# Performance work log

Hardware: AMD Instinct MI355X
Metric: run time of the kernel (lower is better)

The kernel has to match this reference:

```python
import jax, jax.numpy as jnp
import numpy as np

DIM = 64


def setup_inputs() -> dict:
    key = jax.random.key(0)
    k1, k2, k3 = jax.random.split(key, 3)
    x = jax.random.normal(k1, (65536, DIM), dtype=jnp.float32)
    alpha = jax.random.uniform(k2, (), dtype=jnp.float32)
    beta = jax.random.uniform(k3, (), dtype=jnp.float32)
    return {"x": x, "alpha": alpha, "beta": beta}


def reference(x, alpha, beta):
    # Static upper-triangular index pairs (i < j), same as triu(...,1).nonzero()
    iu, ju = jnp.triu_indices(DIM, k=1)
    e = jnp.exp(-alpha * x)                 # [B, dim]
    # a[b, p] = exp(-alpha*x_i) - exp(-alpha*x_j) for each pair p=(i,j), i<j.
    # Equivalent to building the dense [B, dim, dim] tensor and gathering triu.
    a = e[..., iu] - e[..., ju]             # [B, dim*(dim-1)/2]
    log_vander = jnp.sum(jnp.log(jnp.abs(a)), axis=-1)  # [B]
    return 2.0 * (-beta * jnp.sum(x, axis=-1) + log_vander)
```

## Files before the change

kernel.cpp:

```cpp
#include <hip/hip_runtime.h>

#define RS 66

typedef float v2f __attribute__((ext_vector_type(2)));

__device__ __forceinline__ float lgc(float p) {
  return __builtin_amdgcn_logf(__builtin_fmaxf(__builtin_fabsf(p), 1e-37f));
}

__device__ __forceinline__ void ld8v(const float* p, v2f (&r)[4]) {
#pragma unroll
  for (int k = 0; k < 4; ++k) r[k] = *reinterpret_cast<const v2f*>(p + 2 * k);
}

__device__ __forceinline__ void row8p(float a, const v2f (&ej)[4], float& acc) {
  v2f aa = {a, a};
  v2f d0 = aa - ej[0], d1 = aa - ej[1], d2 = aa - ej[2], d3 = aa - ej[3];
  v2f p = (d0 * d1) * (d2 * d3);
  acc += lgc(p.x * p.y);
}

__device__ __forceinline__ void crossp(const v2f (&ei)[4], const v2f (&ej)[4],
                                       float& a0, float& a1) {
  row8p(ei[0].x, ej, a0); row8p(ei[0].y, ej, a1);
  row8p(ei[1].x, ej, a0); row8p(ei[1].y, ej, a1);
  row8p(ei[2].x, ej, a0); row8p(ei[2].y, ej, a1);
  row8p(ei[3].x, ej, a0); row8p(ei[3].y, ej, a1);
}

__device__ __forceinline__ void diag(const v2f (&v)[4], float& a0, float& a1) {
  float e0 = v[0].x, e1 = v[0].y, e2 = v[1].x, e3 = v[1].y;
  float e4 = v[2].x, e5 = v[2].y, e6 = v[3].x, e7 = v[3].y;
  a0 += lgc((((e0 - e1) * (e0 - e2)) * ((e0 - e3) * (e0 - e4))) *
            (((e0 - e5) * (e0 - e6)) * ((e0 - e7) * (e1 - e2))));
  a1 += lgc((((e1 - e3) * (e1 - e4)) * ((e1 - e5) * (e1 - e6))) *
            (((e1 - e7) * (e2 - e3)) * ((e2 - e4) * (e2 - e5))));
  a0 += lgc((((e2 - e6) * (e2 - e7)) * ((e3 - e4) * (e3 - e5))) *
            (((e3 - e6) * (e3 - e7)) * ((e4 - e5) * (e4 - e6))));
  a1 += lgc(((e4 - e7) * (e5 - e6)) * ((e5 - e7) * (e6 - e7)));
}

__global__ __launch_bounds__(512, 8) void vander_kernel(
    const float* __restrict__ x, const float* __restrict__ alpha,
    const float* __restrict__ beta, float* __restrict__ out) {
  __shared__ float e_lds[64 * RS];
  __shared__ float xsum[64 * 9];
  __shared__ float ps[64 * 9];

  const int tid = threadIdx.x;
  const float c = -alpha[0] * 1.44269504088896340736f;

  {
    const int r = tid >> 3, cc = tid & 7;
    const float4* xp = reinterpret_cast<const float4*>(
        x + ((size_t)blockIdx.x * 64 + r) * 64 + cc * 8);
    float4 u = xp[0], v = xp[1];
    float* ew = &e_lds[r * RS + cc * 8];
    float2 t;
    t.x = __builtin_amdgcn_exp2f(c * u.x); t.y = __builtin_amdgcn_exp2f(c * u.y);
    *reinterpret_cast<float2*>(ew + 0) = t;
    t.x = __builtin_amdgcn_exp2f(c * u.z); t.y = __builtin_amdgcn_exp2f(c * u.w);
    *reinterpret_cast<float2*>(ew + 2) = t;
    t.x = __builtin_amdgcn_exp2f(c * v.x); t.y = __builtin_amdgcn_exp2f(c * v.y);
    *reinterpret_cast<float2*>(ew + 4) = t;
    t.x = __builtin_amdgcn_exp2f(c * v.z); t.y = __builtin_amdgcn_exp2f(c * v.w);
    *reinterpret_cast<float2*>(ew + 6) = t;
    xsum[r * 9 + cc] = ((u.x + u.y) + (u.z + u.w)) + ((v.x + v.y) + (v.z + v.w));
  }
  __syncthreads();

  const int lane = tid & 63;
  const int w = tid >> 6;
  const float* myrow = &e_lds[lane * RS];

  v2f ei[4], ej[4];
  ld8v(myrow + w * 8, ei);
  float a0 = 0.f, a1 = 0.f;

  ld8v(myrow + ((w + 1) & 7) * 8, ej);
  crossp(ei, ej, a0, a1);
  ld8v(myrow + ((w + 2) & 7) * 8, ej);
  crossp(ei, ej, a0, a1);
  ld8v(myrow + ((w + 3) & 7) * 8, ej);
  crossp(ei, ej, a0, a1);

  ld8v(myrow + ((w + 4) & 7) * 8, ej);
  if (w < 4) {
    row8p(ei[0].x, ej, a0); row8p(ei[0].y, ej, a1);
    row8p(ei[1].x, ej, a0); row8p(ei[1].y, ej, a1);
  } else {
    row8p(ej[2].x, ei, a0); row8p(ej[2].y, ei, a1);
    row8p(ej[3].x, ei, a0); row8p(ej[3].y, ei, a1);
  }
  diag(ei, a0, a1);

  ps[lane * 9 + w] = a0 + a1;
  __syncthreads();

  if (w == 0) {
    const float* pp = &ps[lane * 9];
    const float* xq = &xsum[lane * 9];
    float lv = ((pp[0] + pp[1]) + (pp[2] + pp[3])) + ((pp[4] + pp[5]) + (pp[6] + pp[7]));
    float xs = ((xq[0] + xq[1]) + (xq[2] + xq[3])) + ((xq[4] + xq[5]) + (xq[6] + xq[7]));
    out[blockIdx.x * 64 + lane] =
        2.0f * (-beta[0] * xs + 0.69314718055994530942f * lv);
  }
}

extern "C" void kernel_launch(void* const* d_in, const int* in_sizes, int n_in,
                              void* d_out, int out_size, void* d_ws, size_t ws_size,
                              hipStream_t stream) {
  const float* x = (const float*)d_in[0];
  const float* alpha = (const float*)d_in[1];
  const float* beta = (const float*)d_in[2];
  float* out = (float*)d_out;
  int nrows = in_sizes[0] / 64;
  int grid = nrows / 64;
  hipLaunchKernelGGL(vander_kernel, dim3(grid), dim3(512), 0, stream,
                     x, alpha, beta, out);
}
```

Before: 71.09 us.

## Replace per-product log with exponent/mantissa accumulation and a single final log

Groups pair differences into 16-element products and accumulates each product's exponent bits as an integer and its mantissa in [1,2) as a running float product. Per thread, only one log2 of the mantissa product is taken at the end, instead of one log per 8-element product. This cuts the transcendental instruction count roughly in half or more and replaces it with cheap integer and bit operations. The trade-offs are that 16-term products can underflow or overflow, which the 1e-37 clamp masks, and that the mantissa product chain (up to about 8 multiplies across two accumulators) may lose precision or overflow.

```diff
diff --git a/kernel.cpp b/kernel.cpp
--- a/kernel.cpp
+++ b/kernel.cpp
@@ -4,8 +4,11 @@
 
 typedef float v2f __attribute__((ext_vector_type(2)));
 
-__device__ __forceinline__ float lgc(float p) {
-  return __builtin_amdgcn_logf(__builtin_fmaxf(__builtin_fabsf(p), 1e-37f));
+__device__ __forceinline__ void acc16(float p, int& ea, float& m) {
+  p = __builtin_fmaxf(__builtin_fabsf(p), 1e-37f);
+  const int b = __float_as_int(p);
+  ea += (b >> 23);
+  m *= __int_as_float((b & 0x007FFFFF) | 0x3F800000);
 }
 
 __device__ __forceinline__ void ld8v(const float* p, v2f (&r)[4]) {
@@ -13,31 +16,37 @@
   for (int k = 0; k < 4; ++k) r[k] = *reinterpret_cast<const v2f*>(p + 2 * k);
 }
 
-__device__ __forceinline__ void row8p(float a, const v2f (&ej)[4], float& acc) {
-  v2f aa = {a, a};
-  v2f d0 = aa - ej[0], d1 = aa - ej[1], d2 = aa - ej[2], d3 = aa - ej[3];
-  v2f p = (d0 * d1) * (d2 * d3);
-  acc += lgc(p.x * p.y);
+__device__ __forceinline__ void row16(float a, float b, const v2f (&ej)[4],
+                                      int& ea, float& m) {
+  v2f aa = {a, a}, bb = {b, b};
+  v2f qa = ((aa - ej[0]) * (aa - ej[1])) * ((aa - ej[2]) * (aa - ej[3]));
+  v2f qb = ((bb - ej[0]) * (bb - ej[1])) * ((bb - ej[2]) * (bb - ej[3]));
+  v2f q = qa * qb;
+  acc16(q.x * q.y, ea, m);
 }
 
 __device__ __forceinline__ void crossp(const v2f (&ei)[4], const v2f (&ej)[4],
-                                       float& a0, float& a1) {
-  row8p(ei[0].x, ej, a0); row8p(ei[0].y, ej, a1);
-  row8p(ei[1].x, ej, a0); row8p(ei[1].y, ej, a1);
-  row8p(ei[2].x, ej, a0); row8p(ei[2].y, ej, a1);
-  row8p(ei[3].x, ej, a0); row8p(ei[3].y, ej, a1);
+                                       int& e0, float& m0, int& e1, float& m1) {
+  row16(ei[0].x, ei[0].y, ej, e0, m0);
+  row16(ei[1].x, ei[1].y, ej, e1, m1);
+  row16(ei[2].x, ei[2].y, ej, e0, m0);
+  row16(ei[3].x, ei[3].y, ej, e1, m1);
 }
 
-__device__ __forceinline__ void diag(const v2f (&v)[4], float& a0, float& a1) {
-  float e0 = v[0].x, e1 = v[0].y, e2 = v[1].x, e3 = v[1].y;
-  float e4 = v[2].x, e5 = v[2].y, e6 = v[3].x, e7 = v[3].y;
-  a0 += lgc((((e0 - e1) * (e0 - e2)) * ((e0 - e3) * (e0 - e4))) *
-            (((e0 - e5) * (e0 - e6)) * ((e0 - e7) * (e1 - e2))));
-  a1 += lgc((((e1 - e3) * (e1 - e4)) * ((e1 - e5) * (e1 - e6))) *
-            (((e1 - e7) * (e2 - e3)) * ((e2 - e4) * (e2 - e5))));
-  a0 += lgc((((e2 - e6) * (e2 - e7)) * ((e3 - e4) * (e3 - e5))) *
-            (((e3 - e6) * (e3 - e7)) * ((e4 - e5) * (e4 - e6))));
-  a1 += lgc(((e4 - e7) * (e5 - e6)) * ((e5 - e7) * (e6 - e7)));
+__device__ __forceinline__ void diag(const v2f (&v)[4], int& e0, float& m0,
+                                     int& e1, float& m1) {
+  float a = v[0].x, b = v[0].y, c = v[1].x, d = v[1].y;
+  float e = v[2].x, f = v[2].y, g = v[3].x, h = v[3].y;
+  float p1 = ((((a - b) * (a - c)) * ((a - d) * (a - e))) *
+              (((a - f) * (a - g)) * ((a - h) * (b - c)))) *
+             ((((b - d) * (b - e)) * ((b - f) * (b - g))) *
+              ((b - h) * (c - d)));
+  acc16(p1, e0, m0);
+  float p2 = ((((c - e) * (c - f)) * ((c - g) * (c - h))) *
+              (((d - e) * (d - f)) * ((d - g) * (d - h)))) *
+             ((((e - f) * (e - g)) * ((e - h) * (f - g))) *
+              ((f - h) * (g - h)));
+  acc16(p2, e1, m1);
 }
 
 __global__ __launch_bounds__(512, 8) void vander_kernel(
@@ -75,35 +84,37 @@
 
   v2f ei[4], ej[4];
   ld8v(myrow + w * 8, ei);
-  float a0 = 0.f, a1 = 0.f;
+  int e0 = 0, e1 = 0;
+  float m0 = 1.f, m1 = 1.f;
 
   ld8v(myrow + ((w + 1) & 7) * 8, ej);
-  crossp(ei, ej, a0, a1);
+  crossp(ei, ej, e0, m0, e1, m1);
   ld8v(myrow + ((w + 2) & 7) * 8, ej);
-  crossp(ei, ej, a0, a1);
+  crossp(ei, ej, e0, m0, e1, m1);
   ld8v(myrow + ((w + 3) & 7) * 8, ej);
-  crossp(ei, ej, a0, a1);
+  crossp(ei, ej, e0, m0, e1, m1);
 
   ld8v(myrow + ((w + 4) & 7) * 8, ej);
   if (w < 4) {
-    row8p(ei[0].x, ej, a0); row8p(ei[0].y, ej, a1);
-    row8p(ei[1].x, ej, a0); row8p(ei[1].y, ej, a1);
+    row16(ei[0].x, ei[0].y, ej, e0, m0);
+    row16(ei[1].x, ei[1].y, ej, e1, m1);
   } else {
-    row8p(ej[2].x, ei, a0); row8p(ej[2].y, ei, a1);
-    row8p(ej[3].x, ei, a0); row8p(ej[3].y, ei, a1);
+    row16(ej[2].x, ej[2].y, ei, e0, m0);
+    row16(ej[3].x, ej[3].y, ei, e1, m1);
   }
-  diag(ei, a0, a1);
+  diag(ei, e0, m0, e1, m1);
 
-  ps[lane * 9 + w] = a0 + a1;
+  float lv = (float)(e0 + e1 - 16 * 127) + __builtin_amdgcn_logf(m0 * m1);
+  ps[lane * 9 + w] = lv;
   __syncthreads();
 
   if (w == 0) {
     const float* pp = &ps[lane * 9];
     const float* xq = &xsum[lane * 9];
-    float lv = ((pp[0] + pp[1]) + (pp[2] + pp[3])) + ((pp[4] + pp[5]) + (pp[6] + pp[7]));
+    float lv2 = ((pp[0] + pp[1]) + (pp[2] + pp[3])) + ((pp[4] + pp[5]) + (pp[6] + pp[7]));
     float xs = ((xq[0] + xq[1]) + (xq[2] + xq[3])) + ((xq[4] + xq[5]) + (xq[6] + xq[7]));
     out[blockIdx.x * 64 + lane] =
-        2.0f * (-beta[0] * xs + 0.69314718055994530942f * lv);
+        2.0f * (-beta[0] * xs + 0.69314718055994530942f * lv2);
   }
 }
 
```

New measurement: 69.92 us. About the same (-1.7%).
